# Kernel optimization log

Measured on AMD Instinct MI355X. Metric: run time of the kernel, lower is better.

## Reference

```python
import jax, jax.numpy as jnp
import numpy as np

B, H, S, D = 2, 16, 2048, 64  # batch, heads, seq_len, depth (F_hidden)
EPS_ADJ = 1e-09
NEG_INF = -1000000000.0


def iswiglu(x):
    # x * silu(x) == x^2 * sigmoid(x), always >= 0
    return x * jax.nn.silu(x)


def setup_inputs() -> dict:
    key = jax.random.key(0)
    ks = jax.random.split(key, 8)
    Hin = jax.random.normal(ks[0], (B, H, S, D), jnp.float32)
    Hk = jax.random.normal(ks[1], (B, H, S, D), jnp.float32)
    Hv = jax.random.normal(ks[2], (B, H, S, D), jnp.float32)
    A = jax.random.normal(ks[3], (B, H, D, D), jnp.float32)
    # causal (look-ahead) mask: 1 where attention is disallowed
    mask = jnp.triu(jnp.ones((S, S), jnp.float32), k=1)[None, None, :, :]
    xavier = np.sqrt(2.0 / (D + D)).astype(np.float32)  # xavier_normal gain=1 for [D,D] fans
    W = jax.random.normal(ks[4], (H, D, D), jnp.float32) * xavier
    pw = jax.random.normal(ks[5], (H, D, D), jnp.float32) * xavier
    a = jax.random.normal(ks[6], (H, D, D), jnp.float32) * xavier
    b = jnp.zeros((H, D, D), jnp.float32)
    ba = jnp.zeros((H, D, D), jnp.float32)
    return {"Hin": Hin, "Hk": Hk, "Hv": Hv, "A": A, "mask": mask,
            "W": W, "b": b, "pw": pw, "a": a, "ba": ba}


def reference(Hin, Hk, Hv, A, mask, W, b, pw, a, ba):
    # metric-tensor transform: AW = iSwiGLU(W @ A + b) + eps   [B,H,D,D]
    x = jnp.einsum('hij,bhjk->bhik', W, A) + b[None]
    AW = iswiglu(x) + EPS_ADJ
    # energy-curvature tensor: avAp = a @ AW**pw + ba           [B,H,D,D]
    Ap = jnp.power(AW, pw[None])
    avAp = jnp.einsum('hij,bhjk->bhik', a, Ap) + ba[None]
    # bilinear attention scores: (Hin @ avAp) @ Hk^T / sqrt(D)  [B,H,S,S]
    q = jnp.matmul(Hin, avAp)
    Ep = jnp.matmul(q, jnp.swapaxes(Hk, -1, -2)) / jnp.sqrt(jnp.float32(D))
    E = jax.nn.softmax(Ep + mask * NEG_INF, axis=-1)
    Hout = jnp.matmul(E, Hv)                                   # [B,H,S,D]
    return Hout
```

## Files before the change

kernel.cpp:

```cpp
#include <hip/hip_runtime.h>


typedef short v8s __attribute__((ext_vector_type(8)));
typedef float v4f __attribute__((ext_vector_type(4)));

__device__ __forceinline__ float bf2f(unsigned short u) {
    union { unsigned int i; float f; } v; v.i = ((unsigned int)u) << 16; return v.f;
}
__device__ __forceinline__ unsigned short f2bf(float f) {
    unsigned int u = __float_as_uint(f);
    u += 0x7fffu + ((u >> 16) & 1u);
    return (unsigned short)(u >> 16);
}
__device__ __forceinline__ v4f mfma16(v8s a, v8s b, v4f c) {
    return __builtin_amdgcn_mfma_f32_16x16x32_bf16(a, b, c, 0, 0, 0);
}
__device__ __forceinline__ void gload_lds16(const void* g, void* l) {
    __builtin_amdgcn_global_load_lds(
        (const __attribute__((address_space(1))) void*)g,
        (__attribute__((address_space(3))) void*)l, 16, 0, 0);
}
__device__ __forceinline__ void block_sync() {
    asm volatile("" ::: "memory");
    __builtin_amdgcn_s_barrier();
    asm volatile("" ::: "memory");
}

__global__ __launch_bounds__(256)
void pre1_kernel(const float* __restrict__ A,  const float* __restrict__ W,
                 const float* __restrict__ b,  const float* __restrict__ pw,
                 float* __restrict__ Pbuf)
{
    __shared__ float sA[4096], sW[512];
    const int bx = blockIdx.x, bh = blockIdx.y, h = bh & 15, t = threadIdx.x;
    const int lcol = t & 63, lrow = t >> 6, r0 = bx * 8;
    for (int i = t; i < 4096; i += 256) sA[i] = A[bh*4096 + i];
    for (int i = t; i < 512;  i += 256) sW[i] = W[h*4096 + r0*64 + i];
    __syncthreads();
    double acc[2];
    #pragma unroll
    for (int e = 0; e < 2; ++e)
        acc[e] = (double)b[h*4096 + (r0 + lrow + 4*e)*64 + lcol];
    #pragma unroll 4
    for (int jj = 0; jj < 16; ++jj) {
        double a0 = (double)sA[(4*jj+0)*64 + lcol];
        double a1 = (double)sA[(4*jj+1)*64 + lcol];
        double a2 = (double)sA[(4*jj+2)*64 + lcol];
        double a3 = (double)sA[(4*jj+3)*64 + lcol];
        #pragma unroll
        for (int e = 0; e < 2; ++e) {
            const float* wr = &sW[(lrow + 4*e)*64 + 4*jj];
            acc[e] += (double)wr[0]*a0 + (double)wr[1]*a1
                    + (double)wr[2]*a2 + (double)wr[3]*a3;
        }
    }
    #pragma unroll
    for (int e = 0; e < 2; ++e) {
        int idx = (r0 + lrow + 4*e)*64 + lcol;
        double v = acc[e];
        double sig = 1.0 / (1.0 + exp(-v));
        Pbuf[bh*4096 + idx] = (float)pow(v*v*sig + 1e-9, (double)pw[h*4096 + idx]);
    }
}

__global__ __launch_bounds__(256)
void pre2_kernel(const float* __restrict__ a,  const float* __restrict__ ba,
                 const float* __restrict__ Pbuf, float* __restrict__ avap)
{
    __shared__ float sP[4096], sa[512];
    const int bx = blockIdx.x, bh = blockIdx.y, h = bh & 15, t = threadIdx.x;
    const int lcol = t & 63, lrow = t >> 6, r0 = bx * 8;
    for (int i = t; i < 4096; i += 256) sP[i] = Pbuf[bh*4096 + i];
    for (int i = t; i < 512;  i += 256) sa[i] = a[h*4096 + r0*64 + i];
    __syncthreads();
    double acc[2];
    #pragma unroll
    for (int e = 0; e < 2; ++e)
        acc[e] = (double)ba[h*4096 + (r0 + lrow + 4*e)*64 + lcol];
    #pragma unroll 4
    for (int jj = 0; jj < 16; ++jj) {
        double a0 = (double)sP[(4*jj+0)*64 + lcol];
        double a1 = (double)sP[(4*jj+1)*64 + lcol];
        double a2 = (double)sP[(4*jj+2)*64 + lcol];
        double a3 = (double)sP[(4*jj+3)*64 + lcol];
        #pragma unroll
        for (int e = 0; e < 2; ++e) {
            const float* wr = &sa[(lrow + 4*e)*64 + 4*jj];
            acc[e] += (double)wr[0]*a0 + (double)wr[1]*a1
                    + (double)wr[2]*a2 + (double)wr[3]*a3;
        }
    }
    #pragma unroll
    for (int e = 0; e < 2; ++e)
        avap[bh*4096 + (r0 + lrow + 4*e)*64 + lcol] = (float)acc[e];
}

__global__ __launch_bounds__(256)
void pre_legacy(const float* __restrict__ A,  const float* __restrict__ W,
                const float* __restrict__ b,  const float* __restrict__ pw,
                const float* __restrict__ a,  const float* __restrict__ ba,
                float* __restrict__ avap)
{
    __shared__ float sW[4096], sA[4096], sP[4096];
    const int bh = blockIdx.x, h = bh & 15, t = threadIdx.x;
    const int lcol = t & 63, lrow = t >> 6;
    for (int i = t; i < 4096; i += 256) { sW[i] = W[h*4096+i]; sA[i] = A[bh*4096+i]; }
    __syncthreads();
    {
        double acc[16];
        #pragma unroll
        for (int e = 0; e < 16; ++e)
            acc[e] = (double)b[h*4096 + (lrow + 4*e)*64 + lcol];
        #pragma unroll 4
        for (int jj = 0; jj < 16; ++jj) {
            double a0 = (double)sA[(4*jj+0)*64 + lcol];
            double a1 = (double)sA[(4*jj+1)*64 + lcol];
            double a2 = (double)sA[(4*jj+2)*64 + lcol];
            double a3 = (double)sA[(4*jj+3)*64 + lcol];
            #pragma unroll
            for (int e = 0; e < 16; ++e) {
                const float* wr = &sW[(lrow + 4*e)*64 + 4*jj];
                acc[e] += (double)wr[0]*a0 + (double)wr[1]*a1
                        + (double)wr[2]*a2 + (double)wr[3]*a3;
            }
        }
        #pragma unroll
        for (int e = 0; e < 16; ++e) {
            int idx = (lrow + 4*e)*64 + lcol;
            double v = acc[e];
            double sig = 1.0 / (1.0 + exp(-v));
            sP[idx] = (float)pow(v*v*sig + 1e-9, (double)pw[h*4096 + idx]);
        }
    }
    __syncthreads();
    for (int i = t; i < 4096; i += 256) sW[i] = a[h*4096+i];
    __syncthreads();
    {
        double acc[16];
        #pragma unroll
        for (int e = 0; e < 16; ++e)
            acc[e] = (double)ba[h*4096 + (lrow + 4*e)*64 + lcol];
        #pragma unroll 4
        for (int jj = 0; jj < 16; ++jj) {
            double a0 = (double)sP[(4*jj+0)*64 + lcol];
            double a1 = (double)sP[(4*jj+1)*64 + lcol];
            double a2 = (double)sP[(4*jj+2)*64 + lcol];
            double a3 = (double)sP[(4*jj+3)*64 + lcol];
            #pragma unroll
            for (int e = 0; e < 16; ++e) {
                const float* wr = &sW[(lrow + 4*e)*64 + 4*jj];
                acc[e] += (double)wr[0]*a0 + (double)wr[1]*a1
                        + (double)wr[2]*a2 + (double)wr[3]*a3;
            }
        }
        #pragma unroll
        for (int e = 0; e < 16; ++e)
            avap[bh*4096 + (lrow + 4*e)*64 + lcol] = (float)acc[e];
    }
}

__global__ __launch_bounds__(256)
void q_kernel(const float* __restrict__ Hin, const float* __restrict__ avap,
              float* __restrict__ qout)
{
    __shared__ float sH[4096], sAv[4096];
    const int qt = blockIdx.x, bh = blockIdx.y, t = threadIdx.x;
    const int lcol = t & 63, lrow = t >> 6;
    const int base = bh*131072 + qt*4096;
    for (int i = t; i < 4096; i += 256) { sH[i] = Hin[base+i]; sAv[i] = avap[bh*4096+i]; }
    __syncthreads();
    float acc[16];
    #pragma unroll
    for (int e = 0; e < 16; ++e) acc[e] = 0.0f;
    #pragma unroll 4
    for (int jj = 0; jj < 16; ++jj) {
        float a0 = sAv[(4*jj+0)*64 + lcol];
        float a1 = sAv[(4*jj+1)*64 + lcol];
        float a2 = sAv[(4*jj+2)*64 + lcol];
        float a3 = sAv[(4*jj+3)*64 + lcol];
        #pragma unroll
        for (int e = 0; e < 16; ++e) {
            const float* hr = &sH[(lrow + 4*e)*64 + 4*jj];
            acc[e] += hr[0]*a0 + hr[1]*a1 + hr[2]*a2 + hr[3]*a3;
        }
    }
    #pragma unroll
    for (int e = 0; e < 16; ++e)
        qout[base + (lrow + 4*e)*64 + lcol] = acc[e] * 0.125f;
}

__global__ __launch_bounds__(256)
void kvprep_kernel(const float* __restrict__ Hk, const float* __restrict__ Hv,
                   unsigned short* __restrict__ kv)
{
    __shared__ __align__(16) unsigned short sVT[4608];
    const int kt = blockIdx.x, bh = blockIdx.y, t = threadIdx.x;
    const float* hk = Hk + bh*131072 + kt*4096;
    const float* hv = Hv + bh*131072 + kt*4096;
    unsigned short* dst = kv + (size_t)(bh*32 + kt) * 13824;

    #pragma unroll
    for (int it = 0; it < 2; ++it) {
        int item = t + 256*it;
        int kr = item >> 3, oc = item & 7;
        const float* src = hk + kr*64 + oc*8;
        float4 f0 = *(const float4*)(src);
        float4 f1 = *(const float4*)(src + 4);
        float fv[8] = {f0.x,f0.y,f0.z,f0.w,f1.x,f1.y,f1.z,f1.w};
        v8s hi, lo;
        #pragma unroll
        for (int j = 0; j < 8; ++j) {
            unsigned short h = f2bf(fv[j]);
            hi[j] = (short)h;
            lo[j] = (short)f2bf(fv[j] - bf2f(h));
        }
        *(v8s*)(dst + kr*72 + oc*8)        = hi;
        *(v8s*)(dst + 4608 + kr*72 + oc*8) = lo;
    }
    #pragma unroll
    for (int i = 0; i < 16; ++i) {
        int p = t + 256*i;
        int kr = p >> 6, d = p & 63;
        sVT[d*72 + kr] = f2bf(hv[p]);
    }
    __syncthreads();
    const uint4* s4 = (const uint4*)sVT;
    uint4* d4 = (uint4*)(dst + 9216);
    for (int i = t; i < 576; i += 256) d4[i] = s4[i];
}

__global__ __launch_bounds__(256, 2)
void attn_kernel(const unsigned short* __restrict__ kv, float* __restrict__ io)
{
    __shared__ __align__(16) unsigned short sm16[32256];
    const int t    = threadIdx.x;
    const int w    = t >> 6;
    const int lane = t & 63;
    const int l15  = lane & 15;
    const int quad = lane >> 4;
    const int x    = blockIdx.x;
    const int bh   = blockIdx.y;
    const int bhb  = bh * 131072;
    const char* kvb = (const char*)kv + (size_t)bh * 32 * 27648;

    for (int pass = 0; pass < 2; ++pass) {
        const int qt = pass ? (31 - x) : x;
        const int q0 = qt * 64;

        {
            #pragma unroll
            for (int j = 0; j < 7; ++j) {
                int c = w*7 + j;
                if (c < 27)
                    gload_lds16(kvb + c*1024 + (size_t)lane*16, (char*)sm16 + c*1024);
            }
        }

        v8s qhi[2], qlo[2];
        {
            const float* qrow = io + bhb + (q0 + 16*w + l15)*64 + quad*8;
            #pragma unroll
            for (int ks = 0; ks < 2; ++ks)
                #pragma unroll
                for (int j = 0; j < 8; ++j) {
                    float qv = qrow[32*ks + j];
                    unsigned short h = f2bf(qv);
                    unsigned short l = f2bf(qv - bf2f(h));
                    qhi[ks][j] = (short)h; qlo[ks][j] = (short)l;
                }
        }

        v4f O[4];
        float m_[4], l_[4];
        #pragma unroll
        for (int i = 0; i < 4; ++i) { O[i] = (v4f){0,0,0,0}; m_[i] = -1e30f; l_[i] = 0.0f; }

        for (int kt = 0; kt <= qt; ++kt) {
            const int base = (kt & 1) * 13824;
            if (kt < qt) {
                const char* gs = kvb + (size_t)(kt+1) * 27648;
                char* lb = (char*)sm16 + ((kt+1) & 1) * 27648;
                #pragma unroll
                for (int j = 0; j < 7; ++j) {
                    int c = w*7 + j;
                    if (c < 27)
                        gload_lds16(gs + c*1024 + (size_t)lane*16, lb + c*1024);
                }
                if (w < 3) asm volatile("s_waitcnt vmcnt(7)" ::: "memory");
                else       asm volatile("s_waitcnt vmcnt(6)" ::: "memory");
            } else {
                asm volatile("s_waitcnt vmcnt(0)" ::: "memory");
            }
            block_sync();

            v4f s[4];
            #pragma unroll
            for (int ct = 0; ct < 4; ++ct) {
                const unsigned short* kb = &sm16[base + (16*ct + l15)*72 + quad*8];
                v8s kh0 = *(const v8s*)(kb);
                v8s kh1 = *(const v8s*)(kb + 32);
                v8s kl0 = *(const v8s*)(kb + 4608);
                v8s kl1 = *(const v8s*)(kb + 4608 + 32);
                v4f a = (v4f){0,0,0,0};
                a = mfma16(qlo[0], kh0, a);
                a = mfma16(qlo[1], kh1, a);
                a = mfma16(qhi[0], kl0, a);
                a = mfma16(qhi[1], kl1, a);
                a = mfma16(qhi[0], kh0, a);
                a = mfma16(qhi[1], kh1, a);
                s[ct] = a;
            }

            if (kt == qt) {
                #pragma unroll
                for (int ct = 0; ct < 4; ++ct)
                    #pragma unroll
                    for (int r = 0; r < 4; ++r)
                        if (16*ct + l15 > 16*w + quad*4 + r) s[ct][r] = -1e30f;
            }

            float pv[4][4];
            #pragma unroll
            for (int reg = 0; reg < 4; ++reg) {
                float rm = fmaxf(fmaxf(s[0][reg], s[1][reg]), fmaxf(s[2][reg], s[3][reg]));
                rm = fmaxf(rm, __shfl_xor(rm, 1));
                rm = fmaxf(rm, __shfl_xor(rm, 2));
                rm = fmaxf(rm, __shfl_xor(rm, 4));
                rm = fmaxf(rm, __shfl_xor(rm, 8));
                float mn = fmaxf(m_[reg], rm);
                float al = __expf(m_[reg] - mn);
                m_[reg] = mn;
                float rs = 0.0f;
                #pragma unroll
                for (int ct = 0; ct < 4; ++ct) {
                    float e = __expf(s[ct][reg] - mn);
                    pv[ct][reg] = e; rs += e;
                }
                rs += __shfl_xor(rs, 1);
                rs += __shfl_xor(rs, 2);
                rs += __shfl_xor(rs, 4);
                rs += __shfl_xor(rs, 8);
                l_[reg] = l_[reg]*al + rs;
                #pragma unroll
                for (int d = 0; d < 4; ++d) O[d][reg] *= al;
            }

            #pragma unroll
            for (int reg = 0; reg < 4; ++reg)
                #pragma unroll
                for (int ct = 0; ct < 4; ++ct)
                    sm16[27648 + w*1152 + (quad*4+reg)*72 + 16*ct + l15] = f2bf(pv[ct][reg]);
            asm volatile("s_waitcnt lgkmcnt(0)" ::: "memory");

            const unsigned short* pb = &sm16[27648 + w*1152 + l15*72 + quad*8];
            v8s pA0 = *(const v8s*)(pb);
            v8s pA1 = *(const v8s*)(pb + 32);
            #pragma unroll
            for (int d = 0; d < 4; ++d) {
                const unsigned short* vb = &sm16[base + 9216 + (16*d + l15)*72 + quad*8];
                v8s v0 = *(const v8s*)(vb);
                v8s v1 = *(const v8s*)(vb + 32);
                O[d] = mfma16(pA0, v0, O[d]);
                O[d] = mfma16(pA1, v1, O[d]);
            }
            asm volatile("s_waitcnt lgkmcnt(0)" ::: "memory");
            block_sync();
        }

        #pragma unroll
        for (int reg = 0; reg < 4; ++reg) {
            float inv = 1.0f / l_[reg];
            int row = q0 + 16*w + quad*4 + reg;
            #pragma unroll
            for (int d = 0; d < 4; ++d)
                io[bhb + row*64 + 16*d + l15] = O[d][reg] * inv;
        }
    }
}

#define KHI 0
#define KLO 4608
#define VTB 9216
#define PB  13824

__global__ __launch_bounds__(256, 4)
void attn_legacy(const float* __restrict__ Hk, const float* __restrict__ Hv,
                 float* __restrict__ io)
{
    __shared__ __align__(16) unsigned short sm16[18432];
    const int t    = threadIdx.x;
    const int w    = t >> 6;
    const int lane = t & 63;
    const int l15  = lane & 15;
    const int quad = lane >> 4;
    const int x    = blockIdx.x;
    const int bh   = blockIdx.y;
    const int bhb  = bh * 131072;

    for (int pass = 0; pass < 2; ++pass) {
        const int qt = pass ? (31 - x) : x;
        const int q0 = qt * 64;

        v8s qhi[2], qlo[2];
        {
            const float* qrow = io + bhb + (q0 + 16*w + l15)*64 + quad*8;
            #pragma unroll
            for (int ks = 0; ks < 2; ++ks)
                #pragma unroll
                for (int j = 0; j < 8; ++j) {
                    float qv = qrow[32*ks + j];
                    unsigned short h = f2bf(qv);
                    unsigned short l = f2bf(qv - bf2f(h));
                    qhi[ks][j] = (short)h; qlo[ks][j] = (short)l;
                }
        }

        v4f O[4];
        float m_[4], l_[4];
        #pragma unroll
        for (int i = 0; i < 4; ++i) { O[i] = (v4f){0,0,0,0}; m_[i] = -1e30f; l_[i] = 0.0f; }

        for (int kt = 0; kt <= qt; ++kt) {
            __syncthreads();
            const int tb = bhb + kt*4096;
            #pragma unroll 4
            for (int i = 0; i < 16; ++i) {
                int p = t + 256*i;
                int kr = p >> 6, d = p & 63;
                float kvv = Hk[tb + p];
                unsigned short h = f2bf(kvv);
                sm16[KHI + kr*72 + d] = h;
                sm16[KLO + kr*72 + d] = f2bf(kvv - bf2f(h));
                sm16[VTB + d*72 + kr] = f2bf(Hv[tb + p]);
            }
            __syncthreads();

            v4f s[4];
            #pragma unroll
            for (int ct = 0; ct < 4; ++ct) {
                const unsigned short* kb = &sm16[(16*ct + l15)*72 + quad*8];
                v8s kh0 = *(const v8s*)(kb + KHI);
                v8s kh1 = *(const v8s*)(kb + KHI + 32);
                v8s kl0 = *(const v8s*)(kb + KLO);
                v8s kl1 = *(const v8s*)(kb + KLO + 32);
                v4f a = (v4f){0,0,0,0};
                a = mfma16(qlo[0], kh0, a);
                a = mfma16(qlo[1], kh1, a);
                a = mfma16(qhi[0], kl0, a);
                a = mfma16(qhi[1], kl1, a);
                a = mfma16(qhi[0], kh0, a);
                a = mfma16(qhi[1], kh1, a);
                s[ct] = a;
            }

            if (kt == qt) {
                #pragma unroll
                for (int ct = 0; ct < 4; ++ct)
                    #pragma unroll
                    for (int r = 0; r < 4; ++r)
                        if (16*ct + l15 > 16*w + quad*4 + r) s[ct][r] = -1e30f;
            }

            float pv[4][4];
            #pragma unroll
            for (int reg = 0; reg < 4; ++reg) {
                float rm = fmaxf(fmaxf(s[0][reg], s[1][reg]), fmaxf(s[2][reg], s[3][reg]));
                rm = fmaxf(rm, __shfl_xor(rm, 1));
                rm = fmaxf(rm, __shfl_xor(rm, 2));
                rm = fmaxf(rm, __shfl_xor(rm, 4));
                rm = fmaxf(rm, __shfl_xor(rm, 8));
                float mn = fmaxf(m_[reg], rm);
                float al = __expf(m_[reg] - mn);
                m_[reg] = mn;
                float rs = 0.0f;
                #pragma unroll
                for (int ct = 0; ct < 4; ++ct) {
                    float e = __expf(s[ct][reg] - mn);
                    pv[ct][reg] = e; rs += e;
                }
                rs += __shfl_xor(rs, 1);
                rs += __shfl_xor(rs, 2);
                rs += __shfl_xor(rs, 4);
                rs += __shfl_xor(rs, 8);
                l_[reg] = l_[reg]*al + rs;
                #pragma unroll
                for (int d = 0; d < 4; ++d) O[d][reg] *= al;
            }

            #pragma unroll
            for (int reg = 0; reg < 4; ++reg)
                #pragma unroll
                for (int ct = 0; ct < 4; ++ct)
                    sm16[PB + w*1152 + (quad*4+reg)*72 + 16*ct + l15] = f2bf(pv[ct][reg]);
            asm volatile("s_waitcnt lgkmcnt(0)" ::: "memory");

            const unsigned short* pb = &sm16[PB + w*1152 + l15*72 + quad*8];
            v8s pA0 = *(const v8s*)(pb);
            v8s pA1 = *(const v8s*)(pb + 32);
            #pragma unroll
            for (int d = 0; d < 4; ++d) {
                const unsigned short* vb = &sm16[VTB + (16*d + l15)*72 + quad*8];
                v8s v0 = *(const v8s*)(vb);
                v8s v1 = *(const v8s*)(vb + 32);
                O[d] = mfma16(pA0, v0, O[d]);
                O[d] = mfma16(pA1, v1, O[d]);
            }
        }

        #pragma unroll
        for (int reg = 0; reg < 4; ++reg) {
            float inv = 1.0f / l_[reg];
            int row = q0 + 16*w + quad*4 + reg;
            #pragma unroll
            for (int d = 0; d < 4; ++d)
                io[bhb + row*64 + 16*d + l15] = O[d][reg] * inv;
        }
        __syncthreads();
    }
}

extern "C" void kernel_launch(void* const* d_in, const int* in_sizes, int n_in,
                              void* d_out, int out_size, void* d_ws, size_t ws_size,
                              hipStream_t stream)
{
    const float* Hin = (const float*)d_in[0];
    const float* Hk  = (const float*)d_in[1];
    const float* Hv  = (const float*)d_in[2];
    const float* A   = (const float*)d_in[3];
    const float* W   = (const float*)d_in[5];
    const float* b   = (const float*)d_in[6];
    const float* pw  = (const float*)d_in[7];
    const float* a   = (const float*)d_in[8];
    const float* ba  = (const float*)d_in[9];
    float* out  = (float*)d_out;
    float* avap = (float*)d_ws;

    const size_t KVOFF = 1u << 20;
    const size_t NEED  = KVOFF + (size_t)1024 * 27648;

    if (ws_size >= NEED) {
        float* Pbuf = (float*)((char*)d_ws + (512u << 10));
        unsigned short* kvb = (unsigned short*)((char*)d_ws + KVOFF);
        pre1_kernel<<<dim3(8, 32), dim3(256), 0, stream>>>(A, W, b, pw, Pbuf);
        pre2_kernel<<<dim3(8, 32), dim3(256), 0, stream>>>(a, ba, Pbuf, avap);
        kvprep_kernel<<<dim3(32, 32), dim3(256), 0, stream>>>(Hk, Hv, kvb);
        q_kernel<<<dim3(32, 32), dim3(256), 0, stream>>>(Hin, avap, out);
        attn_kernel<<<dim3(16, 32), dim3(256), 0, stream>>>(kvb, out);
    } else {
        pre_legacy<<<dim3(32), dim3(256), 0, stream>>>(A, W, b, pw, a, ba, avap);
        q_kernel<<<dim3(32, 32), dim3(256), 0, stream>>>(Hin, avap, out);
        attn_legacy<<<dim3(16, 32), dim3(256), 0, stream>>>(Hk, Hv, out);
    }
}
```

Measured before the change: 234.9 us.

## Run paired query tiles concurrently in 512-thread attention blocks with XOR-swizzled LDS

The attention kernel now launches 512 threads per block. Waves 0-3 handle query tile x and waves 4-7 handle tile 31-x, so both causal halves share one streamed pass over the K/V tiles instead of two sequential passes. K, V^T and P tiles use an XOR-swizzled 64-wide layout in place of the padded 72-wide one, which shrinks tile size and the workspace. The fp32 q projection is replaced by a split-bf16 MFMA kernel. The cost is idle waves on the short tile while the long tile finishes, plus a larger LDS footprint per block, which may reduce occupancy.

```diff
diff --git a/kernel.cpp b/kernel.cpp
--- a/kernel.cpp
+++ b/kernel.cpp
@@ -160,6 +160,61 @@
 }
 
 __global__ __launch_bounds__(256)
+void q_mfma(const float* __restrict__ Hin, const float* __restrict__ avap,
+            float* __restrict__ qout)
+{
+    __shared__ __align__(16) unsigned short s[16384];
+    const int qt = blockIdx.x, bh = blockIdx.y, t = threadIdx.x;
+    const int w = t >> 6, lane = t & 63, l15 = lane & 15, quad = lane >> 4;
+    const int base = bh*131072 + qt*4096;
+    #pragma unroll
+    for (int i = 0; i < 16; ++i) {
+        int p = t + 256*i;
+        int r = p >> 6, k = p & 63;
+        float v = Hin[base + p];
+        unsigned short h = f2bf(v);
+        int addr = r*64 + (((((k>>3) ^ (r&7))) << 3) | (k & 7));
+        s[addr] = h;
+        s[4096 + addr] = f2bf(v - bf2f(h));
+    }
+    #pragma unroll
+    for (int i = 0; i < 16; ++i) {
+        int p = t + 256*i;
+        int k = p >> 6, n = p & 63;
+        float v = avap[bh*4096 + p];
+        unsigned short h = f2bf(v);
+        int addr = n*64 + (((((k>>3) ^ (n&7))) << 3) | (k & 7));
+        s[8192 + addr] = h;
+        s[12288 + addr] = f2bf(v - bf2f(h));
+    }
+    __syncthreads();
+    const int sl = (quad ^ (l15 & 7)) << 3;
+    const int aoff = (16*w + l15)*64 + sl;
+    v8s ahi0 = *(const v8s*)&s[aoff];
+    v8s ahi1 = *(const v8s*)&s[aoff ^ 32];
+    v8s alo0 = *(const v8s*)&s[4096 + aoff];
+    v8s alo1 = *(const v8s*)&s[4096 + (aoff ^ 32)];
+    #pragma unroll
+    for (int nt = 0; nt < 4; ++nt) {
+        const int boff = 8192 + (16*nt + l15)*64 + sl;
+        v8s bhi0 = *(const v8s*)&s[boff];
+        v8s bhi1 = *(const v8s*)&s[boff ^ 32];
+        v8s blo0 = *(const v8s*)&s[4096 + boff];
+        v8s blo1 = *(const v8s*)&s[4096 + (boff ^ 32)];
+        v4f acc = (v4f){0,0,0,0};
+        acc = mfma16(alo0, bhi0, acc);
+        acc = mfma16(alo1, bhi1, acc);
+        acc = mfma16(ahi0, blo0, acc);
+        acc = mfma16(ahi1, blo1, acc);
+        acc = mfma16(ahi0, bhi0, acc);
+        acc = mfma16(ahi1, bhi1, acc);
+        #pragma unroll
+        for (int reg = 0; reg < 4; ++reg)
+            qout[base + (16*w + quad*4 + reg)*64 + 16*nt + l15] = acc[reg] * 0.125f;
+    }
+}
+
+__global__ __launch_bounds__(256)
 void q_kernel(const float* __restrict__ Hin, const float* __restrict__ avap,
               float* __restrict__ qout)
 {
@@ -193,20 +248,20 @@
 void kvprep_kernel(const float* __restrict__ Hk, const float* __restrict__ Hv,
                    unsigned short* __restrict__ kv)
 {
-    __shared__ __align__(16) unsigned short sVT[4608];
+    __shared__ __align__(16) unsigned short sVT[4096];
     const int kt = blockIdx.x, bh = blockIdx.y, t = threadIdx.x;
     const float* hk = Hk + bh*131072 + kt*4096;
     const float* hv = Hv + bh*131072 + kt*4096;
-    unsigned short* dst = kv + (size_t)(bh*32 + kt) * 13824;
+    unsigned short* dst = kv + (size_t)(bh*32 + kt) * 12288;
 
     #pragma unroll
     for (int it = 0; it < 2; ++it) {
         int item = t + 256*it;
         int kr = item >> 3, oc = item & 7;
         const float* src = hk + kr*64 + oc*8;
-        float4 f0 = *(const float4*)(src);
-        float4 f1 = *(const float4*)(src + 4);
-        float fv[8] = {f0.x,f0.y,f0.z,f0.w,f1.x,f1.y,f1.z,f1.w};
+        float4 g0 = *(const float4*)(src);
+        float4 g1 = *(const float4*)(src + 4);
+        float fv[8] = {g0.x,g0.y,g0.z,g0.w,g1.x,g1.y,g1.z,g1.w};
         v8s hi, lo;
         #pragma unroll
         for (int j = 0; j < 8; ++j) {
@@ -214,93 +269,100 @@
             hi[j] = (short)h;
             lo[j] = (short)f2bf(fv[j] - bf2f(h));
         }
-        *(v8s*)(dst + kr*72 + oc*8)        = hi;
-        *(v8s*)(dst + 4608 + kr*72 + oc*8) = lo;
+        int addr = kr*64 + ((oc ^ (kr & 7)) << 3);
+        *(v8s*)(dst + addr) = hi;
+        *(v8s*)(dst + 4096 + addr) = lo;
     }
     #pragma unroll
     for (int i = 0; i < 16; ++i) {
         int p = t + 256*i;
         int kr = p >> 6, d = p & 63;
-        sVT[d*72 + kr] = f2bf(hv[p]);
-    }
-    __syncthreads();
-    const uint4* s4 = (const uint4*)sVT;
-    uint4* d4 = (uint4*)(dst + 9216);
-    for (int i = t; i < 576; i += 256) d4[i] = s4[i];
-}
-
-__global__ __launch_bounds__(256, 2)
+        sVT[d*64 + (((((kr>>3) ^ (d&7))) << 3) | (kr & 7))] = f2bf(hv[p]);
+    }
+    __syncthreads();
+    #pragma unroll
+    for (int i = 0; i < 2; ++i)
+        ((uint4*)(dst + 8192))[t + 256*i] = ((const uint4*)sVT)[t + 256*i];
+}
+
+#define TILE_HW 12288
+#define PBASE   24576
+
+__global__ __launch_bounds__(512, 4)
 void attn_kernel(const unsigned short* __restrict__ kv, float* __restrict__ io)
 {
-    __shared__ __align__(16) unsigned short sm16[32256];
+    __shared__ __align__(16) unsigned short sm16[32768];
     const int t    = threadIdx.x;
     const int w    = t >> 6;
+    const int wq   = w & 3;
     const int lane = t & 63;
     const int l15  = lane & 15;
     const int quad = lane >> 4;
     const int x    = blockIdx.x;
     const int bh   = blockIdx.y;
     const int bhb  = bh * 131072;
-    const char* kvb = (const char*)kv + (size_t)bh * 32 * 27648;
-
-    for (int pass = 0; pass < 2; ++pass) {
-        const int qt = pass ? (31 - x) : x;
-        const int q0 = qt * 64;
-
-        {
-            #pragma unroll
-            for (int j = 0; j < 7; ++j) {
-                int c = w*7 + j;
-                if (c < 27)
-                    gload_lds16(kvb + c*1024 + (size_t)lane*16, (char*)sm16 + c*1024);
-            }
-        }
-
-        v8s qhi[2], qlo[2];
-        {
-            const float* qrow = io + bhb + (q0 + 16*w + l15)*64 + quad*8;
-            #pragma unroll
-            for (int ks = 0; ks < 2; ++ks)
-                #pragma unroll
-                for (int j = 0; j < 8; ++j) {
-                    float qv = qrow[32*ks + j];
-                    unsigned short h = f2bf(qv);
-                    unsigned short l = f2bf(qv - bf2f(h));
-                    qhi[ks][j] = (short)h; qlo[ks][j] = (short)l;
-                }
-        }
-
-        v4f O[4];
-        float m_[4], l_[4];
-        #pragma unroll
-        for (int i = 0; i < 4; ++i) { O[i] = (v4f){0,0,0,0}; m_[i] = -1e30f; l_[i] = 0.0f; }
-
-        for (int kt = 0; kt <= qt; ++kt) {
-            const int base = (kt & 1) * 13824;
-            if (kt < qt) {
-                const char* gs = kvb + (size_t)(kt+1) * 27648;
-                char* lb = (char*)sm16 + ((kt+1) & 1) * 27648;
-                #pragma unroll
-                for (int j = 0; j < 7; ++j) {
-                    int c = w*7 + j;
-                    if (c < 27)
-                        gload_lds16(gs + c*1024 + (size_t)lane*16, lb + c*1024);
-                }
-                if (w < 3) asm volatile("s_waitcnt vmcnt(7)" ::: "memory");
-                else       asm volatile("s_waitcnt vmcnt(6)" ::: "memory");
-            } else {
-                asm volatile("s_waitcnt vmcnt(0)" ::: "memory");
-            }
-            block_sync();
-
+    const int qt_a = x, qt_b = 31 - x;
+    const int qsel = (w < 4) ? qt_a : qt_b;
+    const int q0   = qsel * 64;
+    const char* kvb = (const char*)(kv + (size_t)bh * 32 * TILE_HW);
+
+    const float* qrow = io + bhb + (q0 + 16*wq + l15)*64 + quad*8;
+    float4 f0 = *(const float4*)(qrow);
+    float4 f1 = *(const float4*)(qrow + 4);
+    float4 f2 = *(const float4*)(qrow + 32);
+    float4 f3 = *(const float4*)(qrow + 36);
+
+    #pragma unroll
+    for (int j = 0; j < 3; ++j) {
+        int c = 3*w + j;
+        gload_lds16(kvb + c*1024 + (size_t)lane*16, (char*)sm16 + c*1024);
+    }
+
+    v8s qhi[2], qlo[2];
+    {
+        float fv0[8] = {f0.x,f0.y,f0.z,f0.w,f1.x,f1.y,f1.z,f1.w};
+        float fv1[8] = {f2.x,f2.y,f2.z,f2.w,f3.x,f3.y,f3.z,f3.w};
+        #pragma unroll
+        for (int j = 0; j < 8; ++j) {
+            unsigned short h0 = f2bf(fv0[j]);
+            qhi[0][j] = (short)h0; qlo[0][j] = (short)f2bf(fv0[j] - bf2f(h0));
+            unsigned short h1 = f2bf(fv1[j]);
+            qhi[1][j] = (short)h1; qlo[1][j] = (short)f2bf(fv1[j] - bf2f(h1));
+        }
+    }
+
+    v4f O[4];
+    float m_[4], l_[4];
+    #pragma unroll
+    for (int i = 0; i < 4; ++i) { O[i] = (v4f){0,0,0,0}; m_[i] = -1e30f; l_[i] = 0.0f; }
+
+    const int sl = (quad ^ (l15 & 7)) << 3;
+
+    for (int kt = 0; kt <= qt_b; ++kt) {
+        const int base = (kt & 1) * TILE_HW;
+        if (kt < qt_b) {
+            const char* gs = kvb + (size_t)(kt+1) * (TILE_HW*2);
+            char* lb = (char*)sm16 + ((kt+1) & 1) * (TILE_HW*2);
+            #pragma unroll
+            for (int j = 0; j < 3; ++j) {
+                int c = 3*w + j;
+                gload_lds16(gs + c*1024 + (size_t)lane*16, lb + c*1024);
+            }
+            asm volatile("s_waitcnt vmcnt(3)" ::: "memory");
+        } else {
+            asm volatile("s_waitcnt vmcnt(0)" ::: "memory");
+        }
+        block_sync();
+
+        if (kt <= qsel) {
             v4f s[4];
             #pragma unroll
             for (int ct = 0; ct < 4; ++ct) {
-                const unsigned short* kb = &sm16[base + (16*ct + l15)*72 + quad*8];
-                v8s kh0 = *(const v8s*)(kb);
-                v8s kh1 = *(const v8s*)(kb + 32);
-                v8s kl0 = *(const v8s*)(kb + 4608);
-                v8s kl1 = *(const v8s*)(kb + 4608 + 32);
+                const int kb = base + (16*ct + l15)*64 + sl;
+                v8s kh0 = *(const v8s*)&sm16[kb];
+                v8s kh1 = *(const v8s*)&sm16[kb ^ 32];
+                v8s kl0 = *(const v8s*)&sm16[kb + 4096];
+                v8s kl1 = *(const v8s*)&sm16[(kb ^ 32) + 4096];
                 v4f a = (v4f){0,0,0,0};
                 a = mfma16(qlo[0], kh0, a);
                 a = mfma16(qlo[1], kh1, a);
@@ -311,12 +373,12 @@
                 s[ct] = a;
             }
 
-            if (kt == qt) {
+            if (kt == qsel) {
                 #pragma unroll
                 for (int ct = 0; ct < 4; ++ct)
                     #pragma unroll
                     for (int r = 0; r < 4; ++r)
-                        if (16*ct + l15 > 16*w + quad*4 + r) s[ct][r] = -1e30f;
+                        if (16*ct + l15 > 16*wq + quad*4 + r) s[ct][r] = -1e30f;
             }
 
             float pv[4][4];
@@ -346,35 +408,39 @@
             }
 
             #pragma unroll
-            for (int reg = 0; reg < 4; ++reg)
+            for (int reg = 0; reg < 4; ++reg) {
+                const int row = quad*4 + reg;
                 #pragma unroll
                 for (int ct = 0; ct < 4; ++ct)
-                    sm16[27648 + w*1152 + (quad*4+reg)*72 + 16*ct + l15] = f2bf(pv[ct][reg]);
+                    sm16[PBASE + w*1024 + row*64 +
+                         ((((2*ct + (l15 >> 3)) ^ (row & 7)) << 3) | (l15 & 7))]
+                        = f2bf(pv[ct][reg]);
+            }
             asm volatile("s_waitcnt lgkmcnt(0)" ::: "memory");
 
-            const unsigned short* pb = &sm16[27648 + w*1152 + l15*72 + quad*8];
-            v8s pA0 = *(const v8s*)(pb);
-            v8s pA1 = *(const v8s*)(pb + 32);
+            const int pb = PBASE + w*1024 + l15*64 + sl;
+            v8s pA0 = *(const v8s*)&sm16[pb];
+            v8s pA1 = *(const v8s*)&sm16[pb ^ 32];
             #pragma unroll
             for (int d = 0; d < 4; ++d) {
-                const unsigned short* vb = &sm16[base + 9216 + (16*d + l15)*72 + quad*8];
-                v8s v0 = *(const v8s*)(vb);
-                v8s v1 = *(const v8s*)(vb + 32);
+                const int vb = base + 8192 + (16*d + l15)*64 + sl;
+                v8s v0 = *(const v8s*)&sm16[vb];
+                v8s v1 = *(const v8s*)&sm16[vb ^ 32];
                 O[d] = mfma16(pA0, v0, O[d]);
                 O[d] = mfma16(pA1, v1, O[d]);
             }
-            asm volatile("s_waitcnt lgkmcnt(0)" ::: "memory");
-            block_sync();
-        }
-
-        #pragma unroll
-        for (int reg = 0; reg < 4; ++reg) {
-            float inv = 1.0f / l_[reg];
-            int row = q0 + 16*w + quad*4 + reg;
-            #pragma unroll
-            for (int d = 0; d < 4; ++d)
-                io[bhb + row*64 + 16*d + l15] = O[d][reg] * inv;
-        }
+        }
+        asm volatile("s_waitcnt lgkmcnt(0)" ::: "memory");
+        block_sync();
+    }
+
+    #pragma unroll
+    for (int reg = 0; reg < 4; ++reg) {
+        float inv = 1.0f / l_[reg];
+        int row = q0 + 16*wq + quad*4 + reg;
+        #pragma unroll
+        for (int d = 0; d < 4; ++d)
+            io[bhb + row*64 + 16*d + l15] = O[d][reg] * inv;
     }
 }
 
@@ -403,12 +469,12 @@
 
         v8s qhi[2], qlo[2];
         {
-            const float* qrow = io + bhb + (q0 + 16*w + l15)*64 + quad*8;
+            const float* qr = io + bhb + (q0 + 16*w + l15)*64 + quad*8;
             #pragma unroll
             for (int ks = 0; ks < 2; ++ks)
                 #pragma unroll
                 for (int j = 0; j < 8; ++j) {
-                    float qv = qrow[32*ks + j];
+                    float qv = qr[32*ks + j];
                     unsigned short h = f2bf(qv);
                     unsigned short l = f2bf(qv - bf2f(h));
                     qhi[ks][j] = (short)h; qlo[ks][j] = (short)l;
@@ -536,7 +602,7 @@
     float* avap = (float*)d_ws;
 
     const size_t KVOFF = 1u << 20;
-    const size_t NEED  = KVOFF + (size_t)1024 * 27648;
+    const size_t NEED  = KVOFF + (size_t)1024 * 24576;
 
     if (ws_size >= NEED) {
         float* Pbuf = (float*)((char*)d_ws + (512u << 10));
@@ -544,8 +610,8 @@
         pre1_kernel<<<dim3(8, 32), dim3(256), 0, stream>>>(A, W, b, pw, Pbuf);
         pre2_kernel<<<dim3(8, 32), dim3(256), 0, stream>>>(a, ba, Pbuf, avap);
         kvprep_kernel<<<dim3(32, 32), dim3(256), 0, stream>>>(Hk, Hv, kvb);
-        q_kernel<<<dim3(32, 32), dim3(256), 0, stream>>>(Hin, avap, out);
-        attn_kernel<<<dim3(16, 32), dim3(256), 0, stream>>>(kvb, out);
+        q_mfma<<<dim3(32, 32), dim3(256), 0, stream>>>(Hin, avap, out);
+        attn_kernel<<<dim3(16, 32), dim3(512), 0, stream>>>(kvb, out);
     } else {
         pre_legacy<<<dim3(32), dim3(256), 0, stream>>>(A, W, b, pw, a, ba, avap);
         q_kernel<<<dim3(32, 32), dim3(256), 0, stream>>>(Hin, avap, out);
```

Measured after the change: 212.5 us. 9.5% less time.
